# Kernel tuning notes

Hardware: AMD Instinct MI355X
Metric: run time of the kernel (lower is better)

## Reference

```python
import jax, jax.numpy as jnp
import numpy as np

NUM_HEADS = 8
OUT_DIM = 128
DEPTH = OUT_DIM // NUM_HEADS  # 16


def setup_inputs() -> dict:
    key = jax.random.key(0)
    ks = jax.random.split(key, 6)
    B, N, F_IN = 32, 512, 64
    x = jax.random.normal(ks[0], (B, N, F_IN), dtype=jnp.float32)
    adj = jax.random.uniform(ks[1], (B, N, N), dtype=jnp.float32)
    wq = jax.random.normal(ks[2], (F_IN, OUT_DIM), dtype=jnp.float32) * 0.05
    wk = jax.random.normal(ks[3], (F_IN, OUT_DIM), dtype=jnp.float32) * 0.05
    wv = jax.random.normal(ks[4], (F_IN, OUT_DIM), dtype=jnp.float32) * 0.05
    wo = jax.random.normal(ks[5], (OUT_DIM, OUT_DIM), dtype=jnp.float32) * 0.05
    return {"x": x, "adj": adj, "wq": wq, "wk": wk, "wv": wv, "wo": wo}


def _split_heads(t, B, N):
    # [B, N, out_dim] -> [B, H, N, D]
    return t.reshape(B, N, NUM_HEADS, DEPTH).transpose(0, 2, 1, 3)


def reference(x, adj, wq, wk, wv, wo):
    B, N, _ = x.shape
    q = _split_heads(x @ wq, B, N)  # [B,H,N,D]
    k = _split_heads(x @ wk, B, N)
    v = _split_heads(x @ wv, B, N)
    scale = jnp.sqrt(jnp.float32(DEPTH))
    scores = jnp.einsum("bhnd,bhmd->bhnm", q, k) / scale  # [B,H,N,N]
    attn = jnp.tanh(scores * adj[:, None, :, :])  # mask-multiply + tanh
    h = jnp.einsum("bhnm,bhmd->bhnd", attn, v)  # [B,H,N,D]
    h = h.transpose(0, 2, 1, 3).reshape(B, N, OUT_DIM)
    return jax.nn.relu(h @ wo)
```

## Files before the change

kernel.cpp:

```cpp
#include <hip/hip_runtime.h>


typedef __bf16 bf16x8 __attribute__((ext_vector_type(8)));
typedef __bf16 bf16x4 __attribute__((ext_vector_type(4)));
typedef float  f32x4  __attribute__((ext_vector_type(4)));

#define MFMA16(a, b, c) __builtin_amdgcn_mfma_f32_16x16x32_bf16((a), (b), (c), 0, 0, 0)

__global__ __launch_bounds__(256) void prep_kernel(
    const float* __restrict__ wq, const float* __restrict__ wk,
    const float* __restrict__ wv, const float* __restrict__ wo,
    __bf16* __restrict__ WTb, __bf16* __restrict__ WoTb)
{
    int idx = blockIdx.x * 256 + threadIdx.x;
    if (idx < 6144) {
        int j4 = idx % 96, k = idx / 96, j = j4 * 4;
        const float* w = (j < 128) ? wq : ((j < 256) ? wk : wv);
        f32x4 v = *(const f32x4*)&w[k * 128 + (j & 127)];
#pragma unroll
        for (int e = 0; e < 4; ++e) WTb[(j + e) * 64 + k] = (__bf16)v[e];
    } else if (idx < 6144 + 4096) {
        int i2 = idx - 6144;
        int j4 = i2 % 32, k = i2 / 32, j = j4 * 4;
        f32x4 v = *(const f32x4*)&wo[k * 128 + j];
#pragma unroll
        for (int e = 0; e < 4; ++e) WoTb[(j + e) * 128 + k] = (__bf16)v[e];
    }
}

__global__ __launch_bounds__(256) void qkv_kernel(
    const float* __restrict__ x, const __bf16* __restrict__ WTb,
    __bf16* __restrict__ Qb, __bf16* __restrict__ Kb, __bf16* __restrict__ VT)
{
    const int tid = threadIdx.x, lane = tid & 63, w = tid >> 6;
    const int g = lane >> 4, lr = lane & 15;
    const long R0 = (long)blockIdx.x * 16;
    const int b = (int)(R0 >> 9);
    const int nloc = (int)(R0 & 511) + g * 4;

    bf16x8 af[2];
#pragma unroll
    for (int kk = 0; kk < 2; ++kk) {
        const float* xp = x + (R0 + lr) * 64 + kk * 32 + g * 8;
        f32x4 x0 = *(const f32x4*)xp, x1 = *(const f32x4*)(xp + 4);
        bf16x8 a;
#pragma unroll
        for (int e = 0; e < 4; ++e) { a[e] = (__bf16)x0[e]; a[4 + e] = (__bf16)x1[e]; }
        af[kk] = a;
    }

#pragma unroll 2
    for (int i = 0; i < 6; ++i) {
        const int j0 = (w * 6 + i) * 16;
        f32x4 acc = {0.f, 0.f, 0.f, 0.f};
#pragma unroll
        for (int kk = 0; kk < 2; ++kk) {
            bf16x8 bf = *(const bf16x8*)&WTb[(j0 + lr) * 64 + kk * 32 + g * 8];
            acc = MFMA16(af[kk], bf, acc);
        }
        const int jj = (j0 + lr) & 127, hh = jj >> 4, d = jj & 15;
        const int bh = b * 8 + hh, t = j0 >> 7;
        if (t == 2) {
            bf16x4 pk;
#pragma unroll
            for (int r = 0; r < 4; ++r) pk[r] = (__bf16)acc[r];
            *(bf16x4*)&VT[((long)bh * 16 + d) * 512 + nloc] = pk;
        } else {
            __bf16* dst = t ? Kb : Qb;
#pragma unroll
            for (int r = 0; r < 4; ++r)
                dst[((long)bh * 512 + nloc + r) * 16 + d] = (__bf16)acc[r];
        }
    }
}

__device__ __forceinline__ float tanh_q(float sadj) {
    const float C = 0.7213475204444817f;
    float e = __builtin_amdgcn_exp2f(sadj * C);
    return 1.0f - 2.0f * __builtin_amdgcn_rcpf(e + 1.0f);
}

struct Tile {
    bf16x8 kf0, kf1;
    bf16x4 v0, v1;
    f32x4 a00, a01, a10, a11;
};

__device__ __forceinline__ Tile load_tile(
    int m0, bool gactive, const __bf16* Kbase, int lr, int g,
    const __bf16* Vrow, const char* aRow0, const char* aRow1, int sw)
{
    Tile t;
    t.kf0 = {}; t.kf1 = {};
    if (gactive) {
        t.kf0 = *(const bf16x8*)&Kbase[(m0 + lr) * 16 + g * 8];
        t.kf1 = *(const bf16x8*)&Kbase[(m0 + 16 + lr) * 16 + g * 8];
    }
    t.v0 = *(const bf16x4*)&Vrow[m0 + g * 4];
    t.v1 = *(const bf16x4*)&Vrow[m0 + 16 + g * 4];
    const int c0 = ((m0 + g * 4) * 4) ^ sw;
    const int c1 = ((m0 + 16 + g * 4) * 4) ^ sw;
    t.a00 = *(const f32x4*)(aRow0 + c0);
    t.a01 = *(const f32x4*)(aRow0 + c1);
    t.a10 = *(const f32x4*)(aRow1 + c0);
    t.a11 = *(const f32x4*)(aRow1 + c1);
    return t;
}

__device__ __forceinline__ void compute_tile(
    const Tile& t, bf16x8 qf0, bf16x8 qf1, f32x4& acc0, f32x4& acc1)
{
    const f32x4 z = {0.f, 0.f, 0.f, 0.f};
    f32x4 s00 = MFMA16(t.kf0, qf0, z);
    f32x4 s01 = MFMA16(t.kf1, qf0, z);
    f32x4 s10 = MFMA16(t.kf0, qf1, z);
    f32x4 s11 = MFMA16(t.kf1, qf1, z);
    bf16x8 p0, p1, vf;
#pragma unroll
    for (int r = 0; r < 4; ++r) {
        p0[r]     = (__bf16)tanh_q(s00[r] * t.a00[r]);
        p0[4 + r] = (__bf16)tanh_q(s01[r] * t.a01[r]);
        p1[r]     = (__bf16)tanh_q(s10[r] * t.a10[r]);
        p1[4 + r] = (__bf16)tanh_q(s11[r] * t.a11[r]);
        vf[r]     = t.v0[r];
        vf[4 + r] = t.v1[r];
    }
    acc0 = MFMA16(p0, vf, acc0);
    acc1 = MFMA16(p1, vf, acc1);
}

__global__ __launch_bounds__(512, 4) void attn_kernel(
    const float* __restrict__ adj,
    const __bf16* __restrict__ Qb, const __bf16* __restrict__ Kb,
    const __bf16* __restrict__ VT, __bf16* __restrict__ Hb)
{
    __shared__ __align__(16) float adjL[32][512];

    const int tid  = threadIdx.x;
    const int lane = tid & 63;
    const int h    = tid >> 6;
    const int g    = lane >> 4;
    const int lr   = lane & 15;
    const int b    = blockIdx.y;
    const int n0   = blockIdx.x * 32;
    const int bh   = b * 8 + h;

    const char* strip = (const char*)(adj + ((long)b * 512 + n0) * 512);
    f32x4 tmp[8];
#pragma unroll
    for (int i = 0; i < 8; ++i)
        tmp[i] = *(const f32x4*)(strip + i * 8192 + tid * 16);
#pragma unroll
    for (int i = 0; i < 8; ++i) {
        int o = i * 8192 + tid * 16;
        int row = o >> 11, col = o & 2047;
        *(f32x4*)((char*)adjL + row * 2048 + (col ^ ((row & 7) << 4))) = tmp[i];
    }

    const bool ga = (g < 2);
    bf16x8 qf0 = {}, qf1 = {};
    if (ga) {
        qf0 = *(const bf16x8*)&Qb[((long)bh * 512 + n0 + lr) * 16 + g * 8];
        qf1 = *(const bf16x8*)&Qb[((long)bh * 512 + n0 + 16 + lr) * 16 + g * 8];
    }

    const __bf16* Kbase = Kb + (long)bh * 512 * 16;
    const __bf16* Vrow  = VT + ((long)bh * 16 + lr) * 512;
    const char*   aRow0 = (const char*)adjL + lr * 2048;
    const char*   aRow1 = (const char*)adjL + (16 + lr) * 2048;
    const int     sw    = (lr & 7) << 4;

    __syncthreads();

    f32x4 acc0 = {0.f, 0.f, 0.f, 0.f}, acc1 = {0.f, 0.f, 0.f, 0.f};

    Tile tA = load_tile(0, ga, Kbase, lr, g, Vrow, aRow0, aRow1, sw);
#pragma unroll 1
    for (int t = 0; t < 16; t += 2) {
        Tile tB = load_tile((t + 1) * 32, ga, Kbase, lr, g, Vrow, aRow0, aRow1, sw);
        compute_tile(tA, qf0, qf1, acc0, acc1);
        if (t + 2 < 16)
            tA = load_tile((t + 2) * 32, ga, Kbase, lr, g, Vrow, aRow0, aRow1, sw);
        compute_tile(tB, qf0, qf1, acc0, acc1);
    }

#pragma unroll
    for (int r = 0; r < 4; ++r) {
        Hb[((long)b * 512 + n0 + g * 4 + r) * 128 + h * 16 + lr]      = (__bf16)acc0[r];
        Hb[((long)b * 512 + n0 + 16 + g * 4 + r) * 128 + h * 16 + lr] = (__bf16)acc1[r];
    }
}

__global__ __launch_bounds__(256) void oproj_kernel(
    const __bf16* __restrict__ Hb, const __bf16* __restrict__ WoTb,
    float* __restrict__ out)
{
    const int tid = threadIdx.x, lane = tid & 63, w = tid >> 6;
    const int g = lane >> 4, lr = lane & 15;
    const long R0 = (long)blockIdx.x * 16;

    bf16x8 af[4];
#pragma unroll
    for (int kk = 0; kk < 4; ++kk)
        af[kk] = *(const bf16x8*)&Hb[(R0 + lr) * 128 + kk * 32 + g * 8];

#pragma unroll
    for (int i = 0; i < 2; ++i) {
        const int j0 = w * 32 + i * 16;
        f32x4 acc = {0.f, 0.f, 0.f, 0.f};
#pragma unroll
        for (int kk = 0; kk < 4; ++kk) {
            bf16x8 bf = *(const bf16x8*)&WoTb[(j0 + lr) * 128 + kk * 32 + g * 8];
            acc = MFMA16(af[kk], bf, acc);
        }
#pragma unroll
        for (int r = 0; r < 4; ++r)
            out[(R0 + g * 4 + r) * 128 + j0 + lr] = fmaxf(acc[r], 0.f);
    }
}

extern "C" void kernel_launch(void* const* d_in, const int* in_sizes, int n_in,
                              void* d_out, int out_size, void* d_ws, size_t ws_size,
                              hipStream_t stream) {
    const float* x   = (const float*)d_in[0];
    const float* adj = (const float*)d_in[1];
    const float* wq  = (const float*)d_in[2];
    const float* wk  = (const float*)d_in[3];
    const float* wv  = (const float*)d_in[4];
    const float* wo  = (const float*)d_in[5];
    float* out = (float*)d_out;

    char* wsb = (char*)d_ws;
    __bf16* WTb  = (__bf16*)wsb;
    __bf16* WoTb = (__bf16*)(wsb + 49152);
    __bf16* Qb   = (__bf16*)(wsb + 81920);
    __bf16* Kb   = Qb + 2097152;
    __bf16* VT   = Kb + 2097152;
    __bf16* Hb   = VT + 2097152;

    prep_kernel<<<40, 256, 0, stream>>>(wq, wk, wv, wo, WTb, WoTb);
    qkv_kernel<<<1024, 256, 0, stream>>>(x, WTb, Qb, Kb, VT);
    attn_kernel<<<dim3(16, 32), 512, 0, stream>>>(adj, Qb, Kb, VT, Hb);
    oproj_kernel<<<1024, 256, 0, stream>>>(Hb, WoTb, out);
}
```

Before: 128.5 us.

## Fuse output projection into attention kernel and stage adj as prescaled bf16

The output projection and ReLU move into the attention kernel. Per-head results go through shared memory so each block computes its 32 output rows directly, which removes the Hb round trip and one kernel launch. The adj strip is loaded with nontemporal loads, prescaled by the tanh constant and stored as padded bf16 in LDS, halving shared memory use and LDS read traffic. The block index is remapped so that a batch's K/V are shared across nearby blocks for L2 reuse. The trade-offs are extra bf16 rounding of adj and two additional block syncs.

```diff
diff --git a/kernel.cpp b/kernel.cpp
--- a/kernel.cpp
+++ b/kernel.cpp
@@ -74,54 +74,53 @@
     }
 }
 
-__device__ __forceinline__ float tanh_q(float sadj) {
-    const float C = 0.7213475204444817f;
-    float e = __builtin_amdgcn_exp2f(sadj * C);
+__device__ __forceinline__ float tanh_e(float x) {
+    float e = __builtin_amdgcn_exp2f(x);
     return 1.0f - 2.0f * __builtin_amdgcn_rcpf(e + 1.0f);
 }
 
 struct Tile {
     bf16x8 kf0, kf1;
     bf16x4 v0, v1;
-    f32x4 a00, a01, a10, a11;
 };
 
 __device__ __forceinline__ Tile load_tile(
-    int m0, bool gactive, const __bf16* Kbase, int lr, int g,
-    const __bf16* Vrow, const char* aRow0, const char* aRow1, int sw)
+    int m0, bool ga, const __bf16* Kbase, int lr, int g, const __bf16* Vrow)
 {
     Tile t;
     t.kf0 = {}; t.kf1 = {};
-    if (gactive) {
+    if (ga) {
         t.kf0 = *(const bf16x8*)&Kbase[(m0 + lr) * 16 + g * 8];
         t.kf1 = *(const bf16x8*)&Kbase[(m0 + 16 + lr) * 16 + g * 8];
     }
     t.v0 = *(const bf16x4*)&Vrow[m0 + g * 4];
     t.v1 = *(const bf16x4*)&Vrow[m0 + 16 + g * 4];
-    const int c0 = ((m0 + g * 4) * 4) ^ sw;
-    const int c1 = ((m0 + 16 + g * 4) * 4) ^ sw;
-    t.a00 = *(const f32x4*)(aRow0 + c0);
-    t.a01 = *(const f32x4*)(aRow0 + c1);
-    t.a10 = *(const f32x4*)(aRow1 + c0);
-    t.a11 = *(const f32x4*)(aRow1 + c1);
     return t;
 }
 
 __device__ __forceinline__ void compute_tile(
-    const Tile& t, bf16x8 qf0, bf16x8 qf1, f32x4& acc0, f32x4& acc1)
-{
+    const Tile& t, int m0, bf16x8 qf0, bf16x8 qf1,
+    const __bf16* aR0, const __bf16* aR1, int g,
+    f32x4& acc0, f32x4& acc1)
+{
+    bf16x4 ba00 = *(const bf16x4*)&aR0[m0 + g * 4];
+    bf16x4 ba01 = *(const bf16x4*)&aR0[m0 + 16 + g * 4];
+    bf16x4 ba10 = *(const bf16x4*)&aR1[m0 + g * 4];
+    bf16x4 ba11 = *(const bf16x4*)&aR1[m0 + 16 + g * 4];
+
     const f32x4 z = {0.f, 0.f, 0.f, 0.f};
     f32x4 s00 = MFMA16(t.kf0, qf0, z);
     f32x4 s01 = MFMA16(t.kf1, qf0, z);
     f32x4 s10 = MFMA16(t.kf0, qf1, z);
     f32x4 s11 = MFMA16(t.kf1, qf1, z);
+
     bf16x8 p0, p1, vf;
 #pragma unroll
     for (int r = 0; r < 4; ++r) {
-        p0[r]     = (__bf16)tanh_q(s00[r] * t.a00[r]);
-        p0[4 + r] = (__bf16)tanh_q(s01[r] * t.a01[r]);
-        p1[r]     = (__bf16)tanh_q(s10[r] * t.a10[r]);
-        p1[4 + r] = (__bf16)tanh_q(s11[r] * t.a11[r]);
+        p0[r]     = (__bf16)tanh_e(s00[r] * (float)ba00[r]);
+        p0[4 + r] = (__bf16)tanh_e(s01[r] * (float)ba01[r]);
+        p1[r]     = (__bf16)tanh_e(s10[r] * (float)ba10[r]);
+        p1[4 + r] = (__bf16)tanh_e(s11[r] * (float)ba11[r]);
         vf[r]     = t.v0[r];
         vf[4 + r] = t.v1[r];
     }
@@ -132,29 +131,35 @@
 __global__ __launch_bounds__(512, 4) void attn_kernel(
     const float* __restrict__ adj,
     const __bf16* __restrict__ Qb, const __bf16* __restrict__ Kb,
-    const __bf16* __restrict__ VT, __bf16* __restrict__ Hb)
-{
-    __shared__ __align__(16) float adjL[32][512];
+    const __bf16* __restrict__ VT, const __bf16* __restrict__ WoTb,
+    float* __restrict__ out)
+{
+    __shared__ __align__(16) char smem[33280];
 
     const int tid  = threadIdx.x;
     const int lane = tid & 63;
     const int h    = tid >> 6;
     const int g    = lane >> 4;
     const int lr   = lane & 15;
-    const int b    = blockIdx.y;
-    const int n0   = blockIdx.x * 32;
-    const int bh   = b * 8 + h;
-
-    const char* strip = (const char*)(adj + ((long)b * 512 + n0) * 512);
-    f32x4 tmp[8];
-#pragma unroll
-    for (int i = 0; i < 8; ++i)
-        tmp[i] = *(const f32x4*)(strip + i * 8192 + tid * 16);
+
+    const int l  = blockIdx.x;
+    const int q  = l >> 3;
+    const int b  = (q >> 4) * 8 + (l & 7);
+    const int n0 = (q & 15) * 32;
+    const int bh = b * 8 + h;
+
+    const float C = 0.7213475204444817f;
+    __bf16* adjL = (__bf16*)smem;
+    const float* strip = adj + ((long)b * 512 + n0) * 512;
 #pragma unroll
     for (int i = 0; i < 8; ++i) {
-        int o = i * 8192 + tid * 16;
-        int row = o >> 11, col = o & 2047;
-        *(f32x4*)((char*)adjL + row * 2048 + (col ^ ((row & 7) << 4))) = tmp[i];
+        int o = i * 2048 + tid * 4;
+        f32x4 v = __builtin_nontemporal_load((const f32x4*)(strip + o));
+        int row = o >> 9, col = o & 511;
+        bf16x4 w;
+#pragma unroll
+        for (int e = 0; e < 4; ++e) w[e] = (__bf16)(v[e] * C);
+        *(bf16x4*)&adjL[row * 520 + col] = w;
     }
 
     const bool ga = (g < 2);
@@ -163,59 +168,57 @@
         qf0 = *(const bf16x8*)&Qb[((long)bh * 512 + n0 + lr) * 16 + g * 8];
         qf1 = *(const bf16x8*)&Qb[((long)bh * 512 + n0 + 16 + lr) * 16 + g * 8];
     }
-
     const __bf16* Kbase = Kb + (long)bh * 512 * 16;
     const __bf16* Vrow  = VT + ((long)bh * 16 + lr) * 512;
-    const char*   aRow0 = (const char*)adjL + lr * 2048;
-    const char*   aRow1 = (const char*)adjL + (16 + lr) * 2048;
-    const int     sw    = (lr & 7) << 4;
+    const __bf16* aR0   = adjL + lr * 520;
+    const __bf16* aR1   = adjL + (16 + lr) * 520;
 
     __syncthreads();
 
     f32x4 acc0 = {0.f, 0.f, 0.f, 0.f}, acc1 = {0.f, 0.f, 0.f, 0.f};
 
-    Tile tA = load_tile(0, ga, Kbase, lr, g, Vrow, aRow0, aRow1, sw);
+    Tile tA = load_tile(0, ga, Kbase, lr, g, Vrow);
 #pragma unroll 1
     for (int t = 0; t < 16; t += 2) {
-        Tile tB = load_tile((t + 1) * 32, ga, Kbase, lr, g, Vrow, aRow0, aRow1, sw);
-        compute_tile(tA, qf0, qf1, acc0, acc1);
+        Tile tB = load_tile((t + 1) * 32, ga, Kbase, lr, g, Vrow);
+        compute_tile(tA, t * 32, qf0, qf1, aR0, aR1, g, acc0, acc1);
         if (t + 2 < 16)
-            tA = load_tile((t + 2) * 32, ga, Kbase, lr, g, Vrow, aRow0, aRow1, sw);
-        compute_tile(tB, qf0, qf1, acc0, acc1);
-    }
-
+            tA = load_tile((t + 2) * 32, ga, Kbase, lr, g, Vrow);
+        compute_tile(tB, (t + 1) * 32, qf0, qf1, aR0, aR1, g, acc0, acc1);
+    }
+
+    __syncthreads();
+    float* hL = (float*)smem;
 #pragma unroll
     for (int r = 0; r < 4; ++r) {
-        Hb[((long)b * 512 + n0 + g * 4 + r) * 128 + h * 16 + lr]      = (__bf16)acc0[r];
-        Hb[((long)b * 512 + n0 + 16 + g * 4 + r) * 128 + h * 16 + lr] = (__bf16)acc1[r];
-    }
-}
-
-__global__ __launch_bounds__(256) void oproj_kernel(
-    const __bf16* __restrict__ Hb, const __bf16* __restrict__ WoTb,
-    float* __restrict__ out)
-{
-    const int tid = threadIdx.x, lane = tid & 63, w = tid >> 6;
-    const int g = lane >> 4, lr = lane & 15;
-    const long R0 = (long)blockIdx.x * 16;
-
-    bf16x8 af[4];
-#pragma unroll
-    for (int kk = 0; kk < 4; ++kk)
-        af[kk] = *(const bf16x8*)&Hb[(R0 + lr) * 128 + kk * 32 + g * 8];
-
-#pragma unroll
-    for (int i = 0; i < 2; ++i) {
-        const int j0 = w * 32 + i * 16;
-        f32x4 acc = {0.f, 0.f, 0.f, 0.f};
-#pragma unroll
-        for (int kk = 0; kk < 4; ++kk) {
-            bf16x8 bf = *(const bf16x8*)&WoTb[(j0 + lr) * 128 + kk * 32 + g * 8];
-            acc = MFMA16(af[kk], bf, acc);
+        hL[(g * 4 + r) * 132 + h * 16 + lr]        = acc0[r];
+        hL[(16 + g * 4 + r) * 132 + h * 16 + lr]   = acc1[r];
+    }
+    __syncthreads();
+
+    f32x4 o0 = {0.f, 0.f, 0.f, 0.f}, o1 = {0.f, 0.f, 0.f, 0.f};
+#pragma unroll
+    for (int kt = 0; kt < 4; ++kt) {
+        bf16x8 wf = *(const bf16x8*)&WoTb[(h * 16 + lr) * 128 + kt * 32 + g * 8];
+        const float* hp0 = &hL[lr * 132 + kt * 32 + g * 8];
+        const float* hp1 = &hL[(16 + lr) * 132 + kt * 32 + g * 8];
+        f32x4 ha = *(const f32x4*)hp0, hb = *(const f32x4*)(hp0 + 4);
+        f32x4 hc = *(const f32x4*)hp1, hd = *(const f32x4*)(hp1 + 4);
+        bf16x8 a0, a1;
+#pragma unroll
+        for (int e = 0; e < 4; ++e) {
+            a0[e] = (__bf16)ha[e]; a0[4 + e] = (__bf16)hb[e];
+            a1[e] = (__bf16)hc[e]; a1[4 + e] = (__bf16)hd[e];
         }
-#pragma unroll
-        for (int r = 0; r < 4; ++r)
-            out[(R0 + g * 4 + r) * 128 + j0 + lr] = fmaxf(acc[r], 0.f);
+        o0 = MFMA16(a0, wf, o0);
+        o1 = MFMA16(a1, wf, o1);
+    }
+
+    const long obase = (long)b * 512 + n0;
+#pragma unroll
+    for (int r = 0; r < 4; ++r) {
+        out[(obase + g * 4 + r) * 128 + h * 16 + lr]      = fmaxf(o0[r], 0.f);
+        out[(obase + 16 + g * 4 + r) * 128 + h * 16 + lr] = fmaxf(o1[r], 0.f);
     }
 }
 
@@ -236,10 +239,8 @@
     __bf16* Qb   = (__bf16*)(wsb + 81920);
     __bf16* Kb   = Qb + 2097152;
     __bf16* VT   = Kb + 2097152;
-    __bf16* Hb   = VT + 2097152;
 
     prep_kernel<<<40, 256, 0, stream>>>(wq, wk, wv, wo, WTb, WoTb);
     qkv_kernel<<<1024, 256, 0, stream>>>(x, WTb, Qb, Kb, VT);
-    attn_kernel<<<dim3(16, 32), 512, 0, stream>>>(adj, Qb, Kb, VT, Hb);
-    oproj_kernel<<<1024, 256, 0, stream>>>(Hb, WoTb, out);
-}
+    attn_kernel<<<512, 512, 0, stream>>>(adj, Qb, Kb, VT, WoTb, out);
+}
```

Result: faster. 124.3 us (-3.3%).
